# Performance work log

Hardware: AMD Instinct MI355X
Metric: run time of the kernel (lower is better)

## Reference

```python
import jax, jax.numpy as jnp
import numpy as np

B, T, M, F, N, H = 2, 1024, 1024, 1024, 16, 64
NEG = -1e30


def _relative_shift(x):
    # x: [b, n, q_len, k_len] -> Transformer-XL pad/reshape shift
    b, h, q_len, k_len = x.shape
    x = jnp.pad(x, ((0, 0), (0, 0), (0, 0), (1, 0)))
    x = x.reshape(b, h, k_len + 1, q_len)[:, :, 1:, :]
    return x.reshape(b, h, q_len, k_len)


def setup_inputs() -> dict:
    key = jax.random.key(0)
    ks = jax.random.split(key, 10)
    std = 0.02
    x = jax.random.normal(ks[0], (B, T, F), jnp.float32)
    rel = jax.random.normal(ks[1], (M + T, F), jnp.float32)
    memory = jax.random.normal(ks[2], (B, M, F), jnp.float32)
    episode_idx = jnp.sort(jax.random.randint(ks[3], (B, M), 0, 4), axis=-1).astype(jnp.int32)
    dones = jax.random.randint(ks[4], (B, T), 0, 2).astype(jnp.int32)
    Wq = jax.random.normal(ks[5], (F, N, H), jnp.float32) * std
    Wk = jax.random.normal(ks[6], (F, N, H), jnp.float32) * std
    Wv = jax.random.normal(ks[7], (F, N, H), jnp.float32) * std
    Wr = jax.random.normal(ks[8], (F, N, H), jnp.float32) * std
    u = jnp.zeros((N, H), jnp.float32)  # bias_init = zeros
    v = jnp.zeros((N, H), jnp.float32)
    Wout = jax.random.normal(ks[9], (N * H, F), jnp.float32) * std
    b_out = jnp.zeros((F,), jnp.float32)
    return {"x": x, "relative_positional_embeddings": rel, "memory": memory,
            "episode_idx": episode_idx, "dones": dones,
            "Wq": Wq, "Wk": Wk, "Wv": Wv, "Wr": Wr, "u": u, "v": v,
            "Wout": Wout, "b_out": b_out}


def reference(x, relative_positional_embeddings, memory, episode_idx, dones,
              Wq, Wk, Wv, Wr, u, v, Wout, b_out):
    scale = 1.0 / np.sqrt(H).astype(np.float32)
    # projections (no bias)
    q = jnp.einsum('btf,fnh->btnh', x, Wq)                      # [B,T,N,H]
    kv_in = jnp.concatenate([memory, x], axis=1)                # [B,M+T,F]
    k = jnp.einsum('bsf,fnh->bsnh', kv_in, Wk)                  # [B,M+T,N,H]
    val = jnp.einsum('bsf,fnh->bsnh', kv_in, Wv)                # [B,M+T,N,H]
    r = jnp.einsum('mf,fnh->mnh', relative_positional_embeddings, Wr)  # [M+T,N,H]

    q_u = q + u[None, None]
    q_v = q + v[None, None]

    # relative positional bias with TXL shift: [B,N,T,M+T]
    bd = jnp.einsum('btnh,mnh->bntm', q_v, r)
    bd = _relative_shift(bd)[..., -(M + T):]
    bias = bd * scale                                           # float32

    # episode mask + causal mask
    qi = episode_idx[:, -1:] + jnp.cumsum(dones, axis=1)        # [B,T]
    ki = jnp.concatenate([episode_idx, qi], axis=1)             # [B,M+T]
    ep_mask = qi[:, None, :, None] == ki[:, None, None, :]      # [B,1,T,M+T]
    causal = jnp.tril(jnp.ones((M + T, M + T), jnp.bool_))[-T:, :][None, None]
    mask = ep_mask & causal                                     # [B,1,T,M+T]

    # attention (matches jax.nn.dot_product_attention XLA path in bf16)
    logits = jnp.einsum('btnh,bsnh->bnts', q_u.astype(jnp.bfloat16), k.astype(jnp.bfloat16))
    logits = logits.astype(jnp.float32) * scale + bias          # [B,N,T,M+T]
    logits = jnp.where(mask, logits, NEG)
    probs = jax.nn.softmax(logits, axis=-1).astype(jnp.bfloat16)
    attn = jnp.einsum('bnts,bsnh->btnh', probs, val.astype(jnp.bfloat16))
    attn = attn.reshape(B, T, N * H).astype(jnp.float32)

    return attn @ Wout + b_out
```

## Files before the change

kernel.cpp:

```cpp
#include <hip/hip_runtime.h>
#include <cstdint>
#include <cstddef>

#define NB 2
#define TT 1024
#define MMEM 1024
#define SS 2048
#define FF 1024
#define NHD 16
#define HD 64

typedef __attribute__((ext_vector_type(8))) short bf16x8;
typedef __attribute__((ext_vector_type(4))) float f32x4;

__device__ __forceinline__ float bf2f(short s){
  unsigned u = ((unsigned)(unsigned short)s) << 16;
  float f; __builtin_memcpy(&f, &u, 4); return f;
}
__device__ __forceinline__ short f2bf(float f){
  unsigned u; __builtin_memcpy(&u, &f, 4);
  u += 0x7fffu + ((u >> 16) & 1u);
  return (short)(u >> 16);
}

typedef const __attribute__((address_space(1))) void gv_t;
typedef __attribute__((address_space(3))) void lv_t;
__device__ __forceinline__ void stage16(const void* g, void* l){
  __builtin_amdgcn_global_load_lds((gv_t*)g, (lv_t*)l, 16, 0, 0);
}


__global__ void build_inputs(const float* __restrict__ mem, const float* __restrict__ x,
                             const float* __restrict__ rel,
                             short* __restrict__ kv, short* __restrict__ relo){
  int i = blockIdx.x * blockDim.x + threadIdx.x;
  const int nkv = NB * SS * FF / 4;
  const float* src; short* dst;
  if (i < nkv){
    int idx = i * 4;
    int row = idx >> 10, col = idx & 1023;
    int b = row >> 11, s = row & 2047;
    src = (s < MMEM) ? (mem + ((size_t)b*MMEM + s)*FF + col)
                     : (x   + ((size_t)b*TT + (s - MMEM))*FF + col);
    dst = kv + (size_t)i * 4;
  } else {
    int j = i - nkv;
    if (j >= SS * FF / 4) return;
    src = rel + (size_t)j * 4;
    dst = relo + (size_t)j * 4;
  }
  float4 v = *(const float4*)src;
  short4 o; o.x = f2bf(v.x); o.y = f2bf(v.y); o.z = f2bf(v.z); o.w = f2bf(v.w);
  *(short4*)dst = o;
}

__global__ void transpose_cast5(const float* __restrict__ i0, const float* __restrict__ i1,
                                const float* __restrict__ i2, const float* __restrict__ i3,
                                const float* __restrict__ i4,
                                short* __restrict__ o0, short* __restrict__ o1,
                                short* __restrict__ o2, short* __restrict__ o3,
                                short* __restrict__ o4){
  const float* in; short* out;
  switch (blockIdx.z){
    case 0: in = i0; out = o0; break;
    case 1: in = i1; out = o1; break;
    case 2: in = i2; out = o2; break;
    case 3: in = i3; out = o3; break;
    default: in = i4; out = o4; break;
  }
  __shared__ float tile[32][33];
  int bx = blockIdx.x * 32, by = blockIdx.y * 32;
  int tx = threadIdx.x, ty = threadIdx.y;
  for (int j = ty; j < 32; j += 8)
    tile[j][tx] = in[(size_t)(by + j)*1024 + bx + tx];
  __syncthreads();
  for (int j = ty; j < 32; j += 8)
    out[(size_t)(bx + j)*1024 + by + tx] = f2bf(tile[tx][j]);
}

__global__ void scan_kernel(const int* __restrict__ episode_idx, const int* __restrict__ dones,
                            int* __restrict__ ki, int2* __restrict__ ranges){
  __shared__ int kis[SS];
  __shared__ int wsum[16];
  const int b = blockIdx.x, t = threadIdx.x;
  const int lane = t & 63, wv = t >> 6;
  int v = dones[b*TT + t];
  kis[t] = episode_idx[b*MMEM + t];
  #pragma unroll
  for (int off = 1; off < 64; off <<= 1){
    int tmp = __shfl_up(v, off, 64);
    if (lane >= off) v += tmp;
  }
  if (lane == 63) wsum[wv] = v;
  __syncthreads();
  int add = 0;
  for (int w = 0; w < wv; w++) add += wsum[w];
  v += add;
  const int base = kis[MMEM - 1];
  const int q = base + v;
  kis[MMEM + t] = q;
  ki[b*SS + t] = kis[t];
  ki[b*SS + MMEM + t] = q;
  __syncthreads();
  if (t < 64){
    const int qlo = kis[MMEM + t*16];
    const int qhi = kis[MMEM + t*16 + 15];
    int lo = 0, hi = SS;
    while (lo < hi){ int mid = (lo + hi) >> 1; if (kis[mid] < qlo) lo = mid + 1; else hi = mid; }
    const int s_lo = lo;
    lo = 0; hi = SS;
    const int tgt = qhi + 1;
    while (lo < hi){ int mid = (lo + hi) >> 1; if (kis[mid] < tgt) lo = mid + 1; else hi = mid; }
    int s_hi = lo;
    const int cap = t*16 + 15 + MMEM + 1;
    if (s_hi > cap) s_hi = cap;
    ranges[(b << 6) + t] = make_int2(s_lo, s_hi);
  }
}

__global__ void bias_tables(const short* __restrict__ kbf, const short* __restrict__ rbf,
                            const float* __restrict__ u, const float* __restrict__ v,
                            float* __restrict__ uk, float* __restrict__ vr){
  int i = blockIdx.x * blockDim.x + threadIdx.x;
  const short* p; const float* w; float* outp;
  if (i < NB * NHD * SS){
    int s = i & 2047, n = (i >> 11) & 15, b = i >> 15;
    p = kbf + (size_t)(b * SS + s) * 1024 + n * 64;
    w = u + n * 64;
    outp = uk + (size_t)(b * NHD + n) * SS + s;
  } else {
    int j = i - NB * NHD * SS;
    if (j >= NHD * SS) return;
    int jj = j & 2047, n = j >> 11;
    p = rbf + (size_t)jj * 1024 + n * 64;
    w = v + n * 64;
    outp = vr + (size_t)n * SS + jj;
  }
  float acc = 0.f;
  #pragma unroll
  for (int c = 0; c < 8; c++){
    bf16x8 kv8 = *(const bf16x8*)(p + c * 8);
    float4 w0 = *(const float4*)(w + c * 8);
    float4 w1 = *(const float4*)(w + c * 8 + 4);
    acc += bf2f(kv8[0])*w0.x + bf2f(kv8[1])*w0.y + bf2f(kv8[2])*w0.z + bf2f(kv8[3])*w0.w
         + bf2f(kv8[4])*w1.x + bf2f(kv8[5])*w1.y + bf2f(kv8[6])*w1.z + bf2f(kv8[7])*w1.w;
  }
  *outp = acc;
}

__device__ __forceinline__ void gemm_core_128x64(const short* __restrict__ A,
                                                 const short* __restrict__ BT,
                                                 int row0, int col0,
                                                 short* As, short* Bs,
                                                 f32x4 (&acc)[4][2]){
  const int tid = threadIdx.x;
  const int lane = tid & 63, wv = tid >> 6;
  const int lcol = lane & 15, quad = lane >> 4;
  const int wr = (wv >> 1) * 64, wc = (wv & 1) * 32;
  const int sw = lcol & 7;
  const int ch0 = (quad ^ sw) * 8;
  const int ch1 = ((4 + quad) ^ sw) * 8;

  #pragma unroll
  for (int r = 0; r < 4; r++)
    #pragma unroll
    for (int c = 0; c < 2; c++) acc[r][c] = (f32x4){0.f, 0.f, 0.f, 0.f};

  const int chk = (tid & 7) ^ ((tid >> 3) & 7);
  const short* gA0 = A  + (size_t)(row0 + (tid >> 3)) * 1024 + chk * 8;
  const short* gB0 = BT + (size_t)(col0 + (tid >> 3)) * 1024 + chk * 8;
  short* dA0 = As + wv * 512;
  short* dB0 = Bs + wv * 512;

  #pragma unroll 1
  for (int k0 = 0; k0 < 1024; k0 += 64){
    __syncthreads();
    #pragma unroll
    for (int j = 0; j < 4; j++)
      stage16(gA0 + (size_t)j * 32768 + k0, dA0 + j * 2048);
    stage16(gB0 + k0, dB0);
    stage16(gB0 + 32768 + k0, dB0 + 2048);
    __syncthreads();
    bf16x8 bfr[2][2];
    #pragma unroll
    for (int c = 0; c < 2; c++){
      const int rb = (wc + c * 16 + lcol) * 64;
      bfr[c][0] = *(const bf16x8*)&Bs[rb + ch0];
      bfr[c][1] = *(const bf16x8*)&Bs[rb + ch1];
    }
    #pragma unroll
    for (int r = 0; r < 4; r++){
      const int rb = (wr + r * 16 + lcol) * 64;
      bf16x8 a0 = *(const bf16x8*)&As[rb + ch0];
      bf16x8 a1 = *(const bf16x8*)&As[rb + ch1];
      #pragma unroll
      for (int c = 0; c < 2; c++){
        acc[r][c] = __builtin_amdgcn_mfma_f32_16x16x32_bf16(a0, bfr[c][0], acc[r][c], 0, 0, 0);
        acc[r][c] = __builtin_amdgcn_mfma_f32_16x16x32_bf16(a1, bfr[c][1], acc[r][c], 0, 0, 0);
      }
    }
  }
}

__global__ __launch_bounds__(256) void proj_gemm(
    const short* __restrict__ kv, const short* __restrict__ relb,
    const short* __restrict__ WkT, const short* __restrict__ WvT,
    const short* __restrict__ WqT, const short* __restrict__ WrT,
    short* __restrict__ kbf, short* __restrict__ vT,
    short* __restrict__ qb, short* __restrict__ rbf,
    const int2* __restrict__ ranges){
  const int z = blockIdx.z;
  const int bx = blockIdx.x;
  const short* A; const short* BT;
  int row0 = bx * 128, qbb = 0;
  if (z == 0 || z == 1){
    const int bb = row0 >> 11;
    const int srow = row0 & 2047;
    if (srow + 128 <= ranges[bb << 6].x) return;
    A = kv; BT = (z == 0) ? WkT : WvT;
  }
  else if (z == 2){
    if (bx >= 16) return;
    qbb = bx >> 3;
    A = kv + (size_t)(qbb * SS + MMEM) * 1024;
    row0 = (bx & 7) * 128;
    BT = WqT;
  }
  else { if (bx >= 16) return; A = relb; BT = WrT; }
  const int col0 = blockIdx.y * 64;

  __shared__ __align__(16) short As[128*64];
  __shared__ __align__(16) short Bs[64*64];
  f32x4 acc[4][2];
  gemm_core_128x64(A, BT, row0, col0, As, Bs, acc);

  const int lane = threadIdx.x & 63, wv = threadIdx.x >> 6;
  const int lcol = lane & 15, quad = lane >> 4;
  const int wr = (wv >> 1) * 64, wc = (wv & 1) * 32;
  #pragma unroll
  for (int c = 0; c < 2; c++){
    const int cc = col0 + wc + c*16 + lcol;
    #pragma unroll
    for (int r = 0; r < 4; r++){
      #pragma unroll
      for (int ri = 0; ri < 4; ri++){
        const int rr = row0 + wr + r*16 + quad*4 + ri;
        float val = acc[r][c][ri];
        if (z == 0){
          kbf[(size_t)rr * 1024 + cc] = f2bf(val);
        } else if (z == 1){
          int b = rr >> 11, s = rr & 2047;
          vT[(size_t)(((b << 4) + (cc >> 6)) * 64 + (cc & 63)) * 2048 + s] = f2bf(val);
        } else if (z == 2){
          qb[((size_t)(qbb * TT) + rr) * 1024 + cc] = f2bf(val);
        } else {
          rbf[(size_t)rr * 1024 + cc] = f2bf(val);
        }
      }
    }
  }
}

__global__ __launch_bounds__(256) void out_gemm(const short* __restrict__ A,
                                                const short* __restrict__ BT,
                                                const float* __restrict__ bias,
                                                float* __restrict__ C){
  const int row0 = blockIdx.x * 128, col0 = blockIdx.y * 64;
  __shared__ __align__(16) short As[128*64];
  __shared__ __align__(16) short Bs[64*64];
  f32x4 acc[4][2];
  gemm_core_128x64(A, BT, row0, col0, As, Bs, acc);

  const int lane = threadIdx.x & 63, wv = threadIdx.x >> 6;
  const int lcol = lane & 15, quad = lane >> 4;
  const int wr = (wv >> 1) * 64, wc = (wv & 1) * 32;
  #pragma unroll
  for (int c = 0; c < 2; c++){
    const int cc = col0 + wc + c*16 + lcol;
    const float bb = bias[cc];
    #pragma unroll
    for (int r = 0; r < 4; r++)
      #pragma unroll
      for (int ri = 0; ri < 4; ri++){
        const int rr = row0 + wr + r*16 + quad*4 + ri;
        C[(size_t)rr * 1024 + cc] = acc[r][c][ri] + bb;
      }
  }
}

__global__ __launch_bounds__(64) void attn_kernel(const short* __restrict__ qb,
                            const short* __restrict__ rbf,
                            const short* __restrict__ kk, const short* __restrict__ vT,
                            const int* __restrict__ ki,
                            const float* __restrict__ uk, const float* __restrict__ vr,
                            const int2* __restrict__ ranges,
                            short* __restrict__ attn_out){
  const int blk = blockIdx.x;
  const int xcd = blk & 7;
  const int idx = blk >> 3;
  const int bn  = (xcd << 2) | (idx >> 6);
  const int t16 = (idx & 63) * 16;
  const int n = bn & 15;
  const int b = bn >> 4;
  const int lane = threadIdx.x & 63;
  const int quad = lane >> 4, lcol = lane & 15;

  __shared__ __align__(16) short pb[16 * 72];

  const short* qp = qb + (size_t)(b * TT + t16 + lcol) * 1024 + n * 64 + quad * 8;
  bf16x8 aq0 = *(const bf16x8*)(qp);
  bf16x8 aq1 = *(const bf16x8*)(qp + 32);

  int trow[4], qi_r[4], sl[4];
  bool hi[4];
  #pragma unroll
  for (int r = 0; r < 4; r++){
    trow[r] = t16 + quad * 4 + r;
    qi_r[r] = ki[b * SS + MMEM + trow[r]];
    const int rt = quad * 4 + r;
    const int off = lcol + 15 - rt;
    sl[r] = quad * 16 + (off & 15);
    hi[r] = off >= 16;
  }

  float m_run[4], l_run[4];
  f32x4 o[4];
  #pragma unroll
  for (int r = 0; r < 4; r++){ m_run[r] = -1e30f; l_run[r] = 0.f; }
  #pragma unroll
  for (int c = 0; c < 4; c++) o[c] = (f32x4){0.f, 0.f, 0.f, 0.f};

  const float scale = 0.125f;
  const size_t vt_base = (size_t)((b * NHD + n) * HD);
  const short* rb_head = rbf + n * 64;
  const float* uk_row = uk + (size_t)(b * NHD + n) * SS;
  const float* vr_row = vr + (size_t)n * SS;

  const int2 rg = ranges[(b << 6) + (t16 >> 4)];
  const int kt0 = rg.x >> 6, kt1 = (rg.y - 1) >> 6;

  for (int kt = kt0; kt <= kt1; kt++){
    const int s0 = kt * 64;
    f32x4 sacc[4];
    float ukc[4];
    #pragma unroll
    for (int c = 0; c < 4; c++){
      const short* kp = kk + (size_t)(b * SS + s0 + 16 * c + lcol) * 1024 + n * 64 + quad * 8;
      bf16x8 b0 = *(const bf16x8*)(kp);
      bf16x8 b1 = *(const bf16x8*)(kp + 32);
      f32x4 z = (f32x4){0.f, 0.f, 0.f, 0.f};
      z = __builtin_amdgcn_mfma_f32_16x16x32_bf16(aq0, b0, z, 0, 0, 0);
      z = __builtin_amdgcn_mfma_f32_16x16x32_bf16(aq1, b1, z, 0, 0, 0);
      sacc[c] = z;
      ukc[c] = uk_row[s0 + 16 * c + lcol];
    }
    int ki_c[4];
    #pragma unroll
    for (int c = 0; c < 4; c++) ki_c[c] = ki[b * SS + s0 + 16 * c + lcol];

    const int j0 = s0 - t16 + 1008;
    f32x4 Dw[5];
    #pragma unroll
    for (int c5 = 0; c5 < 5; c5++){
      int jr = j0 + 16 * c5 + lcol;
      jr = (jr > SS - 1) ? (SS - 1) : jr;
      const short* rp = rb_head + (size_t)jr * 1024 + quad * 8;
      bf16x8 r0 = *(const bf16x8*)(rp);
      bf16x8 r1 = *(const bf16x8*)(rp + 32);
      f32x4 z = (f32x4){0.f, 0.f, 0.f, 0.f};
      z = __builtin_amdgcn_mfma_f32_16x16x32_bf16(aq0, r0, z, 0, 0, 0);
      z = __builtin_amdgcn_mfma_f32_16x16x32_bf16(aq1, r1, z, 0, 0, 0);
      const float vrj = vr_row[jr];
      #pragma unroll
      for (int r = 0; r < 4; r++) z[r] += vrj;
      Dw[c5] = z;
    }

    float p[4][4];
    float rowmax[4];
    #pragma unroll
    for (int r = 0; r < 4; r++) rowmax[r] = -1e30f;
    #pragma unroll
    for (int c = 0; c < 4; c++){
      const int s = s0 + 16 * c + lcol;
      #pragma unroll
      for (int r = 0; r < 4; r++){
        const float v0 = __shfl(Dw[c][r], sl[r], 64);
        const float v1 = __shfl(Dw[c + 1][r], sl[r], 64);
        const float bd = hi[r] ? v1 : v0;
        float lg = (sacc[c][r] + ukc[c] + bd) * scale;
        const bool valid = (s <= trow[r] + MMEM) && (ki_c[c] == qi_r[r]);
        lg = valid ? lg : -1e30f;
        p[c][r] = lg;
        rowmax[r] = fmaxf(rowmax[r], lg);
      }
    }
    #pragma unroll
    for (int r = 0; r < 4; r++){
      float vmx = rowmax[r];
      #pragma unroll
      for (int off = 1; off < 16; off <<= 1) vmx = fmaxf(vmx, __shfl_xor(vmx, off, 64));
      float mnew = fmaxf(m_run[r], vmx);
      float alpha = __expf(m_run[r] - mnew);
      m_run[r] = mnew;
      l_run[r] *= alpha;
      #pragma unroll
      for (int c = 0; c < 4; c++) o[c][r] *= alpha;
    }
    float psum[4] = {0.f, 0.f, 0.f, 0.f};
    #pragma unroll
    for (int c = 0; c < 4; c++)
      #pragma unroll
      for (int r = 0; r < 4; r++){
        float pv = __expf(p[c][r] - m_run[r]);
        p[c][r] = pv;
        psum[r] += pv;
      }
    #pragma unroll
    for (int r = 0; r < 4; r++){
      float vs = psum[r];
      #pragma unroll
      for (int off = 1; off < 16; off <<= 1) vs += __shfl_xor(vs, off, 64);
      l_run[r] += vs;
    }
    #pragma unroll
    for (int c = 0; c < 4; c++)
      #pragma unroll
      for (int r = 0; r < 4; r++)
        pb[(quad * 4 + r) * 72 + 16 * c + lcol] = f2bf(p[c][r]);
    bf16x8 pa0 = *(const bf16x8*)(&pb[lcol * 72 + quad * 8]);
    bf16x8 pa1 = *(const bf16x8*)(&pb[lcol * 72 + 32 + quad * 8]);
    #pragma unroll
    for (int c = 0; c < 4; c++){
      const short* vtp = vT + (vt_base + c * 16 + lcol) * (size_t)SS + s0 + quad * 8;
      bf16x8 bv0 = *(const bf16x8*)(vtp);
      bf16x8 bv1 = *(const bf16x8*)(vtp + 32);
      o[c] = __builtin_amdgcn_mfma_f32_16x16x32_bf16(pa0, bv0, o[c], 0, 0, 0);
      o[c] = __builtin_amdgcn_mfma_f32_16x16x32_bf16(pa1, bv1, o[c], 0, 0, 0);
    }
  }

  #pragma unroll
  for (int r = 0; r < 4; r++){
    const float inv = 1.f / l_run[r];
    const int t = trow[r];
    #pragma unroll
    for (int c = 0; c < 4; c++)
      attn_out[(size_t)(b * TT + t) * 1024 + n * 64 + c * 16 + lcol] = f2bf(o[c][r] * inv);
  }
}

extern "C" void kernel_launch(void* const* d_in, const int* in_sizes, int n_in,
                              void* d_out, int out_size, void* d_ws, size_t ws_size,
                              hipStream_t stream){
  const float* x      = (const float*)d_in[0];
  const float* rel    = (const float*)d_in[1];
  const float* memory = (const float*)d_in[2];
  const int*   episode_idx = (const int*)d_in[3];
  const int*   dones  = (const int*)d_in[4];
  const float* Wq  = (const float*)d_in[5];
  const float* Wk  = (const float*)d_in[6];
  const float* Wv  = (const float*)d_in[7];
  const float* Wr  = (const float*)d_in[8];
  const float* u   = (const float*)d_in[9];
  const float* v   = (const float*)d_in[10];
  const float* Wout  = (const float*)d_in[11];
  const float* b_out = (const float*)d_in[12];
  float* out = (float*)d_out;

  char* ws = (char*)d_ws;
  size_t off = 0;
  auto alloc = [&](size_t bytes) -> char* {
    char* p = ws + off;
    off += (bytes + 255) & ~(size_t)255;
    return p;
  };
  short* kv_bf  = (short*)alloc((size_t)NB * SS * FF * 2);
  short* rel_bf = (short*)alloc((size_t)SS * FF * 2);
  short* WqT    = (short*)alloc((size_t)FF * 1024 * 2);
  short* WkT    = (short*)alloc((size_t)FF * 1024 * 2);
  short* WvT    = (short*)alloc((size_t)FF * 1024 * 2);
  short* WrT    = (short*)alloc((size_t)FF * 1024 * 2);
  short* WoT    = (short*)alloc((size_t)FF * 1024 * 2);
  short* qbuf   = (short*)alloc((size_t)NB * TT * 1024 * 2);
  short* kbf    = (short*)alloc((size_t)NB * SS * 1024 * 2);
  short* vTb    = (short*)alloc((size_t)NB * SS * 1024 * 2);
  short* rbf    = (short*)alloc((size_t)SS * 1024 * 2);
  int*   ki     = (int*)  alloc((size_t)NB * SS * 4);
  int2*  ranges = (int2*) alloc((size_t)NB * 64 * 8);
  float* ukT    = (float*)alloc((size_t)NB * NHD * SS * 4);
  float* vrT    = (float*)alloc((size_t)NHD * SS * 4);
  short* attn   = (short*)alloc((size_t)NB * TT * 1024 * 2);
  (void)ws_size; (void)in_sizes; (void)n_in; (void)out_size;

  const int n4 = NB*SS*FF/4 + SS*FF/4;
  build_inputs<<<(n4 + 255)/256, 256, 0, stream>>>(memory, x, rel, kv_bf, rel_bf);
  dim3 tb(32, 8), tg5(32, 32, 5);
  transpose_cast5<<<tg5, tb, 0, stream>>>(Wq, Wk, Wv, Wr, Wout, WqT, WkT, WvT, WrT, WoT);
  scan_kernel<<<NB, TT, 0, stream>>>(episode_idx, dones, ki, ranges);

  proj_gemm<<<dim3(32, 16, 4), 256, 0, stream>>>(kv_bf, rel_bf,
                                                 WkT, WvT, WqT, WrT,
                                                 kbf, vTb, qbuf, rbf, ranges);

  bias_tables<<<(NB*NHD*SS + NHD*SS + 255)/256, 256, 0, stream>>>(kbf, rbf, u, v, ukT, vrT);

  attn_kernel<<<2048, 64, 0, stream>>>(qbuf, rbf, kbf, vTb, ki, ukT, vrT, ranges, attn);

  out_gemm<<<dim3(16, 16), 256, 0, stream>>>(attn, WoT, b_out, out);
}
```

Baseline: 225.6 us.

## Double-buffer LDS tiles in the shared GEMM core to overlap loads with MFMA

The 128x64 GEMM core used by the projection and output kernels now keeps two LDS buffers for the A and B tiles. It preloads the first k-tile, then stages tile k+1 into the other buffer while running MFMAs on tile k, with one barrier per iteration instead of two. The aim is to hide global-to-LDS latency behind matrix math and drop a barrier. In exchange, LDS per block doubles, which may reduce how many blocks fit on each CU.

```diff
diff --git a/kernel.cpp b/kernel.cpp
--- a/kernel.cpp
+++ b/kernel.cpp
@@ -169,30 +169,44 @@
   const int chk = (tid & 7) ^ ((tid >> 3) & 7);
   const short* gA0 = A  + (size_t)(row0 + (tid >> 3)) * 1024 + chk * 8;
   const short* gB0 = BT + (size_t)(col0 + (tid >> 3)) * 1024 + chk * 8;
-  short* dA0 = As + wv * 512;
-  short* dB0 = Bs + wv * 512;
+
+  {
+    short* dA = As + wv * 512;
+    short* dB = Bs + wv * 512;
+    #pragma unroll
+    for (int j = 0; j < 4; j++)
+      stage16(gA0 + (size_t)j * 32768, dA + j * 2048);
+    stage16(gB0, dB);
+    stage16(gB0 + 32768, dB + 2048);
+  }
 
   #pragma unroll 1
   for (int k0 = 0; k0 < 1024; k0 += 64){
+    const int cur = (k0 >> 6) & 1;
     __syncthreads();
-    #pragma unroll
-    for (int j = 0; j < 4; j++)
-      stage16(gA0 + (size_t)j * 32768 + k0, dA0 + j * 2048);
-    stage16(gB0 + k0, dB0);
-    stage16(gB0 + 32768 + k0, dB0 + 2048);
-    __syncthreads();
+    if (k0 + 64 < 1024){
+      short* dA = As + (cur ^ 1) * 8192 + wv * 512;
+      short* dB = Bs + (cur ^ 1) * 4096 + wv * 512;
+      #pragma unroll
+      for (int j = 0; j < 4; j++)
+        stage16(gA0 + (size_t)j * 32768 + k0 + 64, dA + j * 2048);
+      stage16(gB0 + k0 + 64, dB);
+      stage16(gB0 + 32768 + k0 + 64, dB + 2048);
+    }
+    const short* Ab = As + cur * 8192;
+    const short* Bb = Bs + cur * 4096;
     bf16x8 bfr[2][2];
     #pragma unroll
     for (int c = 0; c < 2; c++){
       const int rb = (wc + c * 16 + lcol) * 64;
-      bfr[c][0] = *(const bf16x8*)&Bs[rb + ch0];
-      bfr[c][1] = *(const bf16x8*)&Bs[rb + ch1];
+      bfr[c][0] = *(const bf16x8*)&Bb[rb + ch0];
+      bfr[c][1] = *(const bf16x8*)&Bb[rb + ch1];
     }
     #pragma unroll
     for (int r = 0; r < 4; r++){
       const int rb = (wr + r * 16 + lcol) * 64;
-      bf16x8 a0 = *(const bf16x8*)&As[rb + ch0];
-      bf16x8 a1 = *(const bf16x8*)&As[rb + ch1];
+      bf16x8 a0 = *(const bf16x8*)&Ab[rb + ch0];
+      bf16x8 a1 = *(const bf16x8*)&Ab[rb + ch1];
       #pragma unroll
       for (int c = 0; c < 2; c++){
         acc[r][c] = __builtin_amdgcn_mfma_f32_16x16x32_bf16(a0, bfr[c][0], acc[r][c], 0, 0, 0);
@@ -229,8 +243,8 @@
   else { if (bx >= 16) return; A = relb; BT = WrT; }
   const int col0 = blockIdx.y * 64;
 
-  __shared__ __align__(16) short As[128*64];
-  __shared__ __align__(16) short Bs[64*64];
+  __shared__ __align__(16) short As[2 * 128 * 64];
+  __shared__ __align__(16) short Bs[2 * 64 * 64];
   f32x4 acc[4][2];
   gemm_core_128x64(A, BT, row0, col0, As, Bs, acc);
 
@@ -266,8 +280,8 @@
                                                 const float* __restrict__ bias,
                                                 float* __restrict__ C){
   const int row0 = blockIdx.x * 128, col0 = blockIdx.y * 64;
-  __shared__ __align__(16) short As[128*64];
-  __shared__ __align__(16) short Bs[64*64];
+  __shared__ __align__(16) short As[2 * 128 * 64];
+  __shared__ __align__(16) short Bs[2 * 64 * 64];
   f32x4 acc[4][2];
   gemm_core_128x64(A, BT, row0, col0, As, Bs, acc);
 
```

Measured after the change: 231.5 us. +2.6%, slower.

## Double-buffer GEMM core with K=32 stages and skip unused relative-embedding tiles

Applied to the files above, without the earlier changes.

Restructures the shared GEMM core into a double-buffered pipeline with 32-wide K slices. The next slice's async global-to-LDS loads are issued before computing the current one, synchronised with explicit vmcnt waits and barriers, and the LDS swizzle is changed to match. It also skips relative-embedding projection tiles whose rows are never referenced, computed from the valid-key ranges. The aim is to hide global load latency behind MFMA work and avoid wasted projection work, at the cost of more barriers per K step and hand-written waitcnt logic.

```diff
diff --git a/kernel.cpp b/kernel.cpp
--- a/kernel.cpp
+++ b/kernel.cpp
@@ -157,48 +157,49 @@
   const int lane = tid & 63, wv = tid >> 6;
   const int lcol = lane & 15, quad = lane >> 4;
   const int wr = (wv >> 1) * 64, wc = (wv & 1) * 32;
-  const int sw = lcol & 7;
-  const int ch0 = (quad ^ sw) * 8;
-  const int ch1 = ((4 + quad) ^ sw) * 8;
+  const int ch = (quad ^ ((lcol >> 1) & 3)) * 8;
 
   #pragma unroll
   for (int r = 0; r < 4; r++)
     #pragma unroll
     for (int c = 0; c < 2; c++) acc[r][c] = (f32x4){0.f, 0.f, 0.f, 0.f};
 
-  const int chk = (tid & 7) ^ ((tid >> 3) & 7);
-  const short* gA0 = A  + (size_t)(row0 + (tid >> 3)) * 1024 + chk * 8;
-  const short* gB0 = BT + (size_t)(col0 + (tid >> 3)) * 1024 + chk * 8;
-  short* dA0 = As + wv * 512;
-  short* dB0 = Bs + wv * 512;
-
-  #pragma unroll 1
-  for (int k0 = 0; k0 < 1024; k0 += 64){
-    __syncthreads();
-    #pragma unroll
-    for (int j = 0; j < 4; j++)
-      stage16(gA0 + (size_t)j * 32768 + k0, dA0 + j * 2048);
-    stage16(gB0 + k0, dB0);
-    stage16(gB0 + 32768 + k0, dB0 + 2048);
-    __syncthreads();
-    bf16x8 bfr[2][2];
-    #pragma unroll
-    for (int c = 0; c < 2; c++){
-      const int rb = (wc + c * 16 + lcol) * 64;
-      bfr[c][0] = *(const bf16x8*)&Bs[rb + ch0];
-      bfr[c][1] = *(const bf16x8*)&Bs[rb + ch1];
-    }
+  const int rA = tid >> 2, pA = tid & 3;
+  const int lA = pA ^ ((rA >> 1) & 3);
+  const short* gA = A  + (size_t)(row0 + rA) * 1024 + lA * 8;
+  const short* gB = BT + (size_t)(col0 + rA) * 1024 + lA * 8;
+  short* dA = As + wv * 512;
+  short* dB = Bs + wv * 512;
+
+  stage16(gA,         dA);
+  stage16(gA + 65536, dA + 2048);
+  stage16(gB,         dB);
+
+  #pragma unroll 2
+  for (int k0 = 0; k0 < 1024; k0 += 32){
+    const int cur = (k0 >> 5) & 1;
+    if (k0 + 32 < 1024){
+      const int nxt = cur ^ 1;
+      stage16(gA + k0 + 32,         As + nxt * 4096 + wv * 512);
+      stage16(gA + 65536 + k0 + 32, As + nxt * 4096 + 2048 + wv * 512);
+      stage16(gB + k0 + 32,         Bs + nxt * 2048 + wv * 512);
+      asm volatile("s_waitcnt vmcnt(3)" ::: "memory");
+    } else {
+      asm volatile("s_waitcnt vmcnt(0)" ::: "memory");
+    }
+    __builtin_amdgcn_s_barrier();
+    const short* Ab = As + cur * 4096;
+    const short* Bb = Bs + cur * 2048;
+    bf16x8 b0 = *(const bf16x8*)&Bb[(wc + lcol) * 32 + ch];
+    bf16x8 b1 = *(const bf16x8*)&Bb[(wc + 16 + lcol) * 32 + ch];
     #pragma unroll
     for (int r = 0; r < 4; r++){
-      const int rb = (wr + r * 16 + lcol) * 64;
-      bf16x8 a0 = *(const bf16x8*)&As[rb + ch0];
-      bf16x8 a1 = *(const bf16x8*)&As[rb + ch1];
-      #pragma unroll
-      for (int c = 0; c < 2; c++){
-        acc[r][c] = __builtin_amdgcn_mfma_f32_16x16x32_bf16(a0, bfr[c][0], acc[r][c], 0, 0, 0);
-        acc[r][c] = __builtin_amdgcn_mfma_f32_16x16x32_bf16(a1, bfr[c][1], acc[r][c], 0, 0, 0);
-      }
-    }
+      bf16x8 a = *(const bf16x8*)&Ab[(wr + r * 16 + lcol) * 32 + ch];
+      acc[r][0] = __builtin_amdgcn_mfma_f32_16x16x32_bf16(a, b0, acc[r][0], 0, 0, 0);
+      acc[r][1] = __builtin_amdgcn_mfma_f32_16x16x32_bf16(a, b1, acc[r][1], 0, 0, 0);
+    }
+    asm volatile("s_waitcnt lgkmcnt(0)" ::: "memory");
+    __builtin_amdgcn_s_barrier();
   }
 }
 
@@ -211,8 +212,10 @@
     const int2* __restrict__ ranges){
   const int z = blockIdx.z;
   const int bx = blockIdx.x;
+  const int tid = threadIdx.x;
   const short* A; const short* BT;
   int row0 = bx * 128, qbb = 0;
+  __shared__ int s_jm;
   if (z == 0 || z == 1){
     const int bb = row0 >> 11;
     const int srow = row0 & 2047;
@@ -226,11 +229,23 @@
     row0 = (bx & 7) * 128;
     BT = WqT;
   }
-  else { if (bx >= 16) return; A = relb; BT = WrT; }
+  else {
+    if (bx >= 16) return;
+    if (tid == 0) s_jm = 0x7fffffff;
+    __syncthreads();
+    if (tid < 128){
+      int2 e = ranges[tid];
+      int jr = (e.x & ~63) - ((tid & 63) << 4) + 1008;
+      atomicMin(&s_jm, jr);
+    }
+    __syncthreads();
+    if (row0 + 128 <= s_jm) return;
+    A = relb; BT = WrT;
+  }
   const int col0 = blockIdx.y * 64;
 
-  __shared__ __align__(16) short As[128*64];
-  __shared__ __align__(16) short Bs[64*64];
+  __shared__ __align__(16) short As[2 * 128 * 32];
+  __shared__ __align__(16) short Bs[2 * 64 * 32];
   f32x4 acc[4][2];
   gemm_core_128x64(A, BT, row0, col0, As, Bs, acc);
 
@@ -266,8 +281,8 @@
                                                 const float* __restrict__ bias,
                                                 float* __restrict__ C){
   const int row0 = blockIdx.x * 128, col0 = blockIdx.y * 64;
-  __shared__ __align__(16) short As[128*64];
-  __shared__ __align__(16) short Bs[64*64];
+  __shared__ __align__(16) short As[2 * 128 * 32];
+  __shared__ __align__(16) short Bs[2 * 64 * 32];
   f32x4 acc[4][2];
   gemm_core_128x64(A, BT, row0, col0, As, Bs, acc);
 
```

Result: slower. 242.0 us (+7.3%).
